# Kernel tuning notes

Hardware: AMD Instinct MI355X
Metric: run time of the kernel (lower is better)

## Reference

```python
import jax, jax.numpy as jnp
import numpy as np

N_NODES = 100000
N_EDGES = 1600000
D = 128

def setup_inputs() -> dict:
    key = jax.random.key(0)
    k1, k2, k3, k4 = jax.random.split(key, 4)
    x = jax.random.normal(k1, (N_NODES, D), dtype=jnp.float32)
    edge_index = jax.random.randint(k2, (2, N_EDGES), 0, N_NODES, dtype=jnp.int64)
    eps = jnp.zeros((1,), dtype=jnp.float32)
    W1 = jax.random.normal(k3, (D, D), dtype=jnp.float32) * (1.0 / np.sqrt(D))
    b1 = jnp.zeros((D,), dtype=jnp.float32)
    W2 = jax.random.normal(k4, (D, D), dtype=jnp.float32) * (1.0 / np.sqrt(D))
    b2 = jnp.zeros((D,), dtype=jnp.float32)
    return {"x": x, "edge_index": edge_index, "eps": eps,
            "W1": W1, "b1": b1, "W2": W2, "b2": b2}

def reference(x, edge_index, eps, W1, b1, W2, b2):
    src, dst = edge_index[0], edge_index[1]
    # spmm: sum of neighbor features h_j for each destination node i
    agg = jax.ops.segment_sum(x[src], dst, num_segments=N_NODES)  # [N, D]
    out = (1.0 + eps[0]) * x + agg
    # apply_func: 2-layer MLP (GIN paper)
    h = jax.nn.relu(out @ W1 + b1)
    return h @ W2 + b2
```

## Files before the change

### kernel.cpp

```cpp
#include <hip/hip_runtime.h>

#define D 128
#define BSHIFT 7
#define NSUB 8
#define SUBCAP 384
#define CAP 2560
#define LDSPITCH 136

#define NBMAX 784
#define LCAP 16
#define FCH 8

typedef __attribute__((ext_vector_type(8))) short bf16x8;
typedef __attribute__((ext_vector_type(4))) float f32x4;
typedef __attribute__((ext_vector_type(2))) float f32x2;
typedef __attribute__((ext_vector_type(4))) unsigned int u32x4;

__device__ __forceinline__ unsigned short f2bf(float f) {
    union { float f; unsigned int u; } c; c.f = f;
    return (unsigned short)((c.u + 0x7FFFu + ((c.u >> 16) & 1u)) >> 16);
}

__global__ __launch_bounds__(256) void conv_all(
    const float* __restrict__ x, unsigned short* __restrict__ xb,
    const float* __restrict__ W1, unsigned short* __restrict__ W1t,
    const float* __restrict__ W2, unsigned short* __restrict__ W2t,
    int* __restrict__ cur, int total4, int ncur)
{
    int gid = blockIdx.x * 256 + threadIdx.x;
    if (gid < total4) {
        float4 v = ((const float4*)x)[gid];
        ushort4 o;
        o.x = f2bf(v.x); o.y = f2bf(v.y); o.z = f2bf(v.z); o.w = f2bf(v.w);
        ((ushort4*)xb)[gid] = o;
        return;
    }
    int r = gid - total4;
    if (r < 16384) {
        int n = r >> 7, k = r & 127;
        W1t[n * 128 + k] = f2bf(W1[k * 128 + n]);
        return;
    }
    r -= 16384;
    if (r < 16384) {
        int n = r >> 7, k = r & 127;
        W2t[n * 128 + k] = f2bf(W2[k * 128 + n]);
        return;
    }
    r -= 16384;
    if (r < ncur) cur[r] = 0;
}

__global__ __launch_bounds__(512) void bin_kernel(
    const int* __restrict__ ei, int* __restrict__ cur,
    int* __restrict__ pairs, int E, int nbuck)
{
    __shared__ int lbuf[NBMAX * LCAP];
    __shared__ int lcnt[NBMAX];

    int tid = threadIdx.x;
    int slice = blockIdx.x & (NSUB - 1);
    int nblocks = gridDim.x;
    int epb = (E + nblocks - 1) / nblocks;
    int start = blockIdx.x * epb;
    int end = min(start + epb, E);

    for (int b = tid; b < nbuck; b += 512) lcnt[b] = 0;
    __syncthreads();

    for (int base = start; base < end; base += 512) {
        int gid = base + tid;
        if (gid < end) {
            int d = __builtin_nontemporal_load(&ei[E + gid]);
            int s = __builtin_nontemporal_load(&ei[gid]);
            int b = d >> BSHIFT;
            int val = ((d & 127) << 17) | s;
            int pos = atomicAdd(&lcnt[b], 1);
            if (pos < LCAP) {
                lbuf[b * LCAP + pos] = val;
            } else {
                int sb = b * NSUB + slice;
                int gp = atomicAdd(&cur[sb], 1);
                if (gp < SUBCAP) pairs[(size_t)sb * SUBCAP + gp] = val;
            }
        }
        __syncthreads();
        for (int b = tid; b < nbuck; b += 512) {
            int c = min(lcnt[b], LCAP);
            int nf = (c / FCH) * FCH;
            if (nf > 0) {
                int sb = b * NSUB + slice;
                int gbase = atomicAdd(&cur[sb], nf);
                int* dst = pairs + (size_t)sb * SUBCAP + gbase;
                if ((gbase & 3) == 0 && gbase + nf <= SUBCAP) {
                    #pragma unroll
                    for (int i = 0; i < LCAP; i += 4) {
                        if (i >= nf) break;
                        *(int4*)(dst + i) = *(int4*)(lbuf + b * LCAP + i);
                    }
                } else {
                    for (int i = 0; i < nf; ++i)
                        if (gbase + i < SUBCAP) dst[i] = lbuf[b * LCAP + i];
                }
                int rem = c - nf;
                for (int i = 0; i < rem; ++i)
                    lbuf[b * LCAP + i] = lbuf[b * LCAP + nf + i];
                lcnt[b] = rem;
            } else {
                lcnt[b] = c;
            }
        }
        __syncthreads();
    }

    for (int b = tid; b < nbuck; b += 512) {
        int c = min(lcnt[b], LCAP);
        if (c > 0) {
            int sb = b * NSUB + slice;
            int gbase = atomicAdd(&cur[sb], c);
            for (int i = 0; i < c; ++i)
                if (gbase + i < SUBCAP)
                    pairs[(size_t)sb * SUBCAP + gbase + i] = lbuf[b * LCAP + i];
        }
    }
}

__global__ __launch_bounds__(256) void local_fill(
    const int* __restrict__ cur, const int* __restrict__ pairs,
    int* __restrict__ csr, int* __restrict__ rs, int N)
{
    __shared__ int ldata[CAP];
    __shared__ int outsrc[CAP];
    __shared__ int lcnt[128], lofs[128], lincl[128];
    __shared__ int red[256];

    int b = blockIdx.x;
    int tid = threadIdx.x;
    int node0 = b << BSHIFT;

    int pacc = 0;
    for (int i = tid; i < b * NSUB; i += 256) pacc += min(cur[i], SUBCAP);
    red[tid] = pacc;
    __syncthreads();
    for (int s = 128; s > 0; s >>= 1) {
        if (tid < s) red[tid] += red[tid + s];
        __syncthreads();
    }
    int base = red[0];

    int off = 0;
    #pragma unroll
    for (int s = 0; s < NSUB; ++s) {
        int c = min(cur[b * NSUB + s], SUBCAP);
        const int* pp = pairs + (size_t)(b * NSUB + s) * SUBCAP;
        for (int i = tid; i < c && off + i < CAP; i += 256)
            ldata[off + i] = pp[i];
        off += c;
    }
    int cnt = min(off, CAP);
    __syncthreads();

    if (tid < 128) lcnt[tid] = 0;
    __syncthreads();
    for (int i = tid; i < cnt; i += 256)
        atomicAdd(&lcnt[ldata[i] >> 17], 1);
    __syncthreads();

    if (tid < 128) lincl[tid] = lcnt[tid];
    __syncthreads();
    for (int off2 = 1; off2 < 128; off2 <<= 1) {
        int t = 0;
        if (tid < 128 && tid >= off2) t = lincl[tid - off2];
        __syncthreads();
        if (tid < 128) lincl[tid] += t;
        __syncthreads();
    }
    if (tid < 128) lofs[tid] = lincl[tid] - lcnt[tid];
    __syncthreads();

    for (int i = tid; i < cnt; i += 256) {
        int v = ldata[i];
        int p = atomicAdd(&lofs[v >> 17], 1);
        outsrc[p] = v & 0x1FFFF;
    }
    __syncthreads();

    for (int i = tid; i < cnt; i += 256)
        csr[base + i] = outsrc[i];
    int nn = N - node0; if (nn > 128) nn = 128;
    if (tid < nn) rs[node0 + tid] = base + lincl[tid];
}

__global__ __launch_bounds__(256) void gather_kernel(
    const unsigned short* __restrict__ xb, const float* __restrict__ epsp,
    const int* __restrict__ rs, const int* __restrict__ csr,
    unsigned short* __restrict__ ub, int N)
{
    int sub  = threadIdx.x >> 5;
    int lane = threadIdx.x & 31;
    int hi   = lane >> 4;
    int c16  = lane & 15;
    int node = blockIdx.x * 8 + sub;
    if (node >= N) return;

    int start = (node == 0) ? 0 : rs[node - 1];
    int end   = rs[node];
    int boff  = c16 * 8;

    f32x2 acc[4];
    {
        float ep1 = 1.0f + epsp[0];
        u32x4 xr = *(const u32x4*)(xb + (size_t)node * D + boff);
        f32x2 z = {0.f, 0.f};
        #pragma unroll
        for (int e = 0; e < 4; ++e) {
            unsigned int w = xr[e];
            f32x2 t;
            t.x = __uint_as_float(w << 16);
            t.y = __uint_as_float(w & 0xFFFF0000u);
            acc[e] = hi ? z : (ep1 * t);
        }
    }

    #define ACC8(v)                                                         \
        {                                                                   \
            _Pragma("unroll")                                               \
            for (int e = 0; e < 4; ++e) {                                   \
                unsigned int w = (v)[e];                                    \
                f32x2 t;                                                    \
                t.x = __uint_as_float(w << 16);                             \
                t.y = __uint_as_float(w & 0xFFFF0000u);                     \
                acc[e] += t;                                                \
            }                                                               \
        }

    int j = start;
    for (; j + 16 <= end; j += 16) {
        int i0 = csr[j      + hi], i1 = csr[j +  2 + hi];
        int i2 = csr[j +  4 + hi], i3 = csr[j +  6 + hi];
        int i4 = csr[j +  8 + hi], i5 = csr[j + 10 + hi];
        int i6 = csr[j + 12 + hi], i7 = csr[j + 14 + hi];
        u32x4 v0 = *(const u32x4*)(xb + (size_t)i0 * D + boff);
        u32x4 v1 = *(const u32x4*)(xb + (size_t)i1 * D + boff);
        u32x4 v2 = *(const u32x4*)(xb + (size_t)i2 * D + boff);
        u32x4 v3 = *(const u32x4*)(xb + (size_t)i3 * D + boff);
        u32x4 v4 = *(const u32x4*)(xb + (size_t)i4 * D + boff);
        u32x4 v5 = *(const u32x4*)(xb + (size_t)i5 * D + boff);
        u32x4 v6 = *(const u32x4*)(xb + (size_t)i6 * D + boff);
        u32x4 v7 = *(const u32x4*)(xb + (size_t)i7 * D + boff);
        ACC8(v0); ACC8(v1); ACC8(v2); ACC8(v3);
        ACC8(v4); ACC8(v5); ACC8(v6); ACC8(v7);
    }
    if (j + 8 <= end) {
        int i0 = csr[j + hi],     i1 = csr[j + 2 + hi];
        int i2 = csr[j + 4 + hi], i3 = csr[j + 6 + hi];
        u32x4 v0 = *(const u32x4*)(xb + (size_t)i0 * D + boff);
        u32x4 v1 = *(const u32x4*)(xb + (size_t)i1 * D + boff);
        u32x4 v2 = *(const u32x4*)(xb + (size_t)i2 * D + boff);
        u32x4 v3 = *(const u32x4*)(xb + (size_t)i3 * D + boff);
        ACC8(v0); ACC8(v1); ACC8(v2); ACC8(v3);
        j += 8;
    }
    if (j < end) {
        int lim = end - 1;
        int e0 = j + hi, e1 = j + 2 + hi, e2 = j + 4 + hi, e3 = j + 6 + hi;
        int s0 = csr[min(e0, lim)], s1 = csr[min(e1, lim)];
        int s2 = csr[min(e2, lim)], s3 = csr[min(e3, lim)];
        u32x4 v0 = *(const u32x4*)(xb + (size_t)s0 * D + boff);
        u32x4 v1 = *(const u32x4*)(xb + (size_t)s1 * D + boff);
        u32x4 v2 = *(const u32x4*)(xb + (size_t)s2 * D + boff);
        u32x4 v3 = *(const u32x4*)(xb + (size_t)s3 * D + boff);
        unsigned int m0 = (e0 < end) ? 0xFFFFFFFFu : 0u;
        unsigned int m1 = (e1 < end) ? 0xFFFFFFFFu : 0u;
        unsigned int m2 = (e2 < end) ? 0xFFFFFFFFu : 0u;
        unsigned int m3 = (e3 < end) ? 0xFFFFFFFFu : 0u;
        #pragma unroll
        for (int e = 0; e < 4; ++e) { v0[e] &= m0; v1[e] &= m1; v2[e] &= m2; v3[e] &= m3; }
        ACC8(v0); ACC8(v1); ACC8(v2); ACC8(v3);
    }
    #undef ACC8

    #pragma unroll
    for (int e = 0; e < 4; ++e) {
        acc[e].x += __shfl_xor(acc[e].x, 16);
        acc[e].y += __shfl_xor(acc[e].y, 16);
    }

    if (hi == 0) {
        u32x4 o;
        #pragma unroll
        for (int e = 0; e < 4; ++e) {
            unsigned int lo = f2bf(acc[e].x);
            unsigned int hf = f2bf(acc[e].y);
            o[e] = lo | (hf << 16);
        }
        __builtin_nontemporal_store(o, (u32x4*)(ub + (size_t)node * D + boff));
    }
}

__global__ __launch_bounds__(256, 2) void mlp_fused(
    const unsigned short* __restrict__ in,
    const unsigned short* __restrict__ W1t, const float* __restrict__ b1,
    const unsigned short* __restrict__ W2t, const float* __restrict__ b2,
    float* __restrict__ out, int N)
{
    __shared__ unsigned short Wl[128 * LDSPITCH];
    __shared__ unsigned short Al[64 * LDSPITCH];

    int tid = threadIdx.x;
    int row0 = blockIdx.x * 64;
    int wave = tid >> 6, lane = tid & 63;
    int l16 = lane & 15, lq = lane >> 4;

    for (int i = tid; i < 128 * 16; i += 256) {
        int r = i >> 4, cc = i & 15;
        ((int4*)(Wl + r * LDSPITCH))[cc] = ((const int4*)(W1t + r * 128))[cc];
    }
    for (int i = tid; i < 64 * 16; i += 256) {
        int r = i >> 4, cc = i & 15;
        int4 v = make_int4(0, 0, 0, 0);
        if (row0 + r < N) v = ((const int4*)(in + (size_t)(row0 + r) * 128))[cc];
        ((int4*)(Al + r * LDSPITCH))[cc] = v;
    }
    __syncthreads();

    f32x4 acc[8];
    #pragma unroll
    for (int t = 0; t < 8; ++t) acc[t] = (f32x4){0.f, 0.f, 0.f, 0.f};

    int arow = wave * 16 + l16;
    #pragma unroll
    for (int kk = 0; kk < 4; ++kk) {
        int k0 = kk * 32 + lq * 8;
        bf16x8 a = *(const bf16x8*)(Al + arow * LDSPITCH + k0);
        #pragma unroll
        for (int t = 0; t < 8; ++t) {
            bf16x8 b = *(const bf16x8*)(Wl + (t * 16 + l16) * LDSPITCH + k0);
            acc[t] = __builtin_amdgcn_mfma_f32_16x16x32_bf16(a, b, acc[t], 0, 0, 0);
        }
    }
    __syncthreads();

    for (int i = tid; i < 128 * 16; i += 256) {
        int r = i >> 4, cc = i & 15;
        ((int4*)(Wl + r * LDSPITCH))[cc] = ((const int4*)(W2t + r * 128))[cc];
    }
    #pragma unroll
    for (int t = 0; t < 8; ++t) {
        int col = t * 16 + l16;
        float bv = b1[col];
        #pragma unroll
        for (int r = 0; r < 4; ++r) {
            int row = wave * 16 + lq * 4 + r;
            float v = fmaxf(acc[t][r] + bv, 0.0f);
            Al[row * LDSPITCH + col] = f2bf(v);
        }
    }
    __syncthreads();

    #pragma unroll
    for (int t = 0; t < 8; ++t) acc[t] = (f32x4){0.f, 0.f, 0.f, 0.f};
    #pragma unroll
    for (int kk = 0; kk < 4; ++kk) {
        int k0 = kk * 32 + lq * 8;
        bf16x8 a = *(const bf16x8*)(Al + arow * LDSPITCH + k0);
        #pragma unroll
        for (int t = 0; t < 8; ++t) {
            bf16x8 b = *(const bf16x8*)(Wl + (t * 16 + l16) * LDSPITCH + k0);
            acc[t] = __builtin_amdgcn_mfma_f32_16x16x32_bf16(a, b, acc[t], 0, 0, 0);
        }
    }

    #pragma unroll
    for (int t = 0; t < 8; ++t) {
        int col = t * 16 + l16;
        float bv = b2[col];
        #pragma unroll
        for (int r = 0; r < 4; ++r) {
            int row = row0 + wave * 16 + lq * 4 + r;
            if (row >= N) continue;
            out[(size_t)row * 128 + col] = acc[t][r] + bv;
        }
    }
}

extern "C" void kernel_launch(void* const* d_in, const int* in_sizes, int n_in,
                              void* d_out, int out_size, void* d_ws, size_t ws_size,
                              hipStream_t stream) {
    const float* x   = (const float*)d_in[0];
    const int*   ei  = (const int*)d_in[1];
    const float* eps = (const float*)d_in[2];
    const float* W1  = (const float*)d_in[3];
    const float* b1  = (const float*)d_in[4];
    const float* W2  = (const float*)d_in[5];
    const float* b2  = (const float*)d_in[6];
    float* out = (float*)d_out;

    int E = in_sizes[1] / 2;
    int N = in_sizes[0] / D;
    int nbuck = (N + 127) >> BSHIFT;
    int ncur = nbuck * NSUB;

    char* ws = (char*)d_ws;
    int* cur   = (int*)(ws);
    int* rs    = (int*)(ws + 32768);
    int* pairs = (int*)(ws + 434176);
    int* csr   = (int*)(ws + 10044416);
    unsigned short* xb  = (unsigned short*)(ws + 16445440);
    unsigned short* ub  = (unsigned short*)(ws + 42046464);
    unsigned short* W1t = (unsigned short*)(ws + 67647488);
    unsigned short* W2t = (unsigned short*)(ws + 67680256);

    int total4 = N * D / 4;
    int convtot = total4 + 32768 + ncur;
    conv_all<<<(convtot + 255) / 256, 256, 0, stream>>>(
        x, xb, W1, W1t, W2, W2t, cur, total4, ncur);

    bin_kernel<<<256, 512, 0, stream>>>(ei, cur, pairs, E, nbuck);
    local_fill<<<nbuck, 256, 0, stream>>>(cur, pairs, csr, rs, N);

    gather_kernel<<<(N + 7) / 8, 256, 0, stream>>>(xb, eps, rs, csr, ub, N);

    int gemm_blocks = (N + 63) / 64;
    mlp_fused<<<gemm_blocks, 256, 0, stream>>>(ub, W1t, b1, W2t, b2, out, N);
}
```

Before: 256.2 us.

## Fuse neighbor gather into MLP kernel and merge conversion with binning

The gather/aggregate stage now runs inside the MLP kernel: each block aggregates its 64 rows directly into LDS, so the bf16 intermediate no longer makes a round trip through global memory and one launch disappears. Separately, the x/weight bf16 conversion blocks are appended to the binning kernel's grid so both run concurrently, and zeroing the cursor array moves into its own tiny kernel. In exchange, the gather loop is unrolled less (8 instead of 16 edges per step), occupancy hints change to 3 blocks per CU, and the MFMA work now waits on serialized per-block gathers.

```diff
diff --git a/kernel.cpp b/kernel.cpp
--- a/kernel.cpp
+++ b/kernel.cpp
@@ -10,6 +10,7 @@
 #define NBMAX 784
 #define LCAP 16
 #define FCH 8
+#define NBIN 256
 
 typedef __attribute__((ext_vector_type(8))) short bf16x8;
 typedef __attribute__((ext_vector_type(4))) float f32x4;
@@ -21,47 +22,54 @@
     return (unsigned short)((c.u + 0x7FFFu + ((c.u >> 16) & 1u)) >> 16);
 }
 
-__global__ __launch_bounds__(256) void conv_all(
+__global__ __launch_bounds__(512) void zerocur(int* __restrict__ cur, int ncur)
+{
+    int gid = blockIdx.x * 512 + threadIdx.x;
+    if (gid < ncur) cur[gid] = 0;
+}
+
+__global__ __launch_bounds__(512) void conv_bin(
     const float* __restrict__ x, unsigned short* __restrict__ xb,
     const float* __restrict__ W1, unsigned short* __restrict__ W1t,
     const float* __restrict__ W2, unsigned short* __restrict__ W2t,
-    int* __restrict__ cur, int total4, int ncur)
-{
-    int gid = blockIdx.x * 256 + threadIdx.x;
-    if (gid < total4) {
-        float4 v = ((const float4*)x)[gid];
-        ushort4 o;
-        o.x = f2bf(v.x); o.y = f2bf(v.y); o.z = f2bf(v.z); o.w = f2bf(v.w);
-        ((ushort4*)xb)[gid] = o;
-        return;
-    }
-    int r = gid - total4;
-    if (r < 16384) {
-        int n = r >> 7, k = r & 127;
-        W1t[n * 128 + k] = f2bf(W1[k * 128 + n]);
-        return;
-    }
-    r -= 16384;
-    if (r < 16384) {
-        int n = r >> 7, k = r & 127;
-        W2t[n * 128 + k] = f2bf(W2[k * 128 + n]);
-        return;
-    }
-    r -= 16384;
-    if (r < ncur) cur[r] = 0;
-}
-
-__global__ __launch_bounds__(512) void bin_kernel(
     const int* __restrict__ ei, int* __restrict__ cur,
-    int* __restrict__ pairs, int E, int nbuck)
+    int* __restrict__ pairs, int E, int nbuck, int total4)
 {
     __shared__ int lbuf[NBMAX * LCAP];
     __shared__ int lcnt[NBMAX];
 
     int tid = threadIdx.x;
+
+    if (blockIdx.x >= NBIN) {
+        int base = (blockIdx.x - NBIN) * 1024 + tid;
+        #pragma unroll
+        for (int t = 0; t < 2; ++t) {
+            int gid = base + t * 512;
+            if (gid < total4) {
+                float4 v = ((const float4*)x)[gid];
+                ushort4 o;
+                o.x = f2bf(v.x); o.y = f2bf(v.y);
+                o.z = f2bf(v.z); o.w = f2bf(v.w);
+                ((ushort4*)xb)[gid] = o;
+            } else {
+                int r = gid - total4;
+                if (r < 16384) {
+                    int n = r >> 7, k = r & 127;
+                    W1t[n * 128 + k] = f2bf(W1[k * 128 + n]);
+                } else {
+                    r -= 16384;
+                    if (r < 16384) {
+                        int n = r >> 7, k = r & 127;
+                        W2t[n * 128 + k] = f2bf(W2[k * 128 + n]);
+                    }
+                }
+            }
+        }
+        return;
+    }
+
     int slice = blockIdx.x & (NSUB - 1);
-    int nblocks = gridDim.x;
-    int epb = (E + nblocks - 1) / nblocks;
+    int epb = (E + NBIN - 1) / NBIN;
     int start = blockIdx.x * epb;
     int end = min(start + epb, E);
 
@@ -191,115 +199,9 @@
     if (tid < nn) rs[node0 + tid] = base + lincl[tid];
 }
 
-__global__ __launch_bounds__(256) void gather_kernel(
+__global__ __launch_bounds__(256, 3) void mlp_gather(
     const unsigned short* __restrict__ xb, const float* __restrict__ epsp,
     const int* __restrict__ rs, const int* __restrict__ csr,
-    unsigned short* __restrict__ ub, int N)
-{
-    int sub  = threadIdx.x >> 5;
-    int lane = threadIdx.x & 31;
-    int hi   = lane >> 4;
-    int c16  = lane & 15;
-    int node = blockIdx.x * 8 + sub;
-    if (node >= N) return;
-
-    int start = (node == 0) ? 0 : rs[node - 1];
-    int end   = rs[node];
-    int boff  = c16 * 8;
-
-    f32x2 acc[4];
-    {
-        float ep1 = 1.0f + epsp[0];
-        u32x4 xr = *(const u32x4*)(xb + (size_t)node * D + boff);
-        f32x2 z = {0.f, 0.f};
-        #pragma unroll
-        for (int e = 0; e < 4; ++e) {
-            unsigned int w = xr[e];
-            f32x2 t;
-            t.x = __uint_as_float(w << 16);
-            t.y = __uint_as_float(w & 0xFFFF0000u);
-            acc[e] = hi ? z : (ep1 * t);
-        }
-    }
-
-    #define ACC8(v)                                                         \
-        {                                                                   \
-            _Pragma("unroll")                                               \
-            for (int e = 0; e < 4; ++e) {                                   \
-                unsigned int w = (v)[e];                                    \
-                f32x2 t;                                                    \
-                t.x = __uint_as_float(w << 16);                             \
-                t.y = __uint_as_float(w & 0xFFFF0000u);                     \
-                acc[e] += t;                                                \
-            }                                                               \
-        }
-
-    int j = start;
-    for (; j + 16 <= end; j += 16) {
-        int i0 = csr[j      + hi], i1 = csr[j +  2 + hi];
-        int i2 = csr[j +  4 + hi], i3 = csr[j +  6 + hi];
-        int i4 = csr[j +  8 + hi], i5 = csr[j + 10 + hi];
-        int i6 = csr[j + 12 + hi], i7 = csr[j + 14 + hi];
-        u32x4 v0 = *(const u32x4*)(xb + (size_t)i0 * D + boff);
-        u32x4 v1 = *(const u32x4*)(xb + (size_t)i1 * D + boff);
-        u32x4 v2 = *(const u32x4*)(xb + (size_t)i2 * D + boff);
-        u32x4 v3 = *(const u32x4*)(xb + (size_t)i3 * D + boff);
-        u32x4 v4 = *(const u32x4*)(xb + (size_t)i4 * D + boff);
-        u32x4 v5 = *(const u32x4*)(xb + (size_t)i5 * D + boff);
-        u32x4 v6 = *(const u32x4*)(xb + (size_t)i6 * D + boff);
-        u32x4 v7 = *(const u32x4*)(xb + (size_t)i7 * D + boff);
-        ACC8(v0); ACC8(v1); ACC8(v2); ACC8(v3);
-        ACC8(v4); ACC8(v5); ACC8(v6); ACC8(v7);
-    }
-    if (j + 8 <= end) {
-        int i0 = csr[j + hi],     i1 = csr[j + 2 + hi];
-        int i2 = csr[j + 4 + hi], i3 = csr[j + 6 + hi];
-        u32x4 v0 = *(const u32x4*)(xb + (size_t)i0 * D + boff);
-        u32x4 v1 = *(const u32x4*)(xb + (size_t)i1 * D + boff);
-        u32x4 v2 = *(const u32x4*)(xb + (size_t)i2 * D + boff);
-        u32x4 v3 = *(const u32x4*)(xb + (size_t)i3 * D + boff);
-        ACC8(v0); ACC8(v1); ACC8(v2); ACC8(v3);
-        j += 8;
-    }
-    if (j < end) {
-        int lim = end - 1;
-        int e0 = j + hi, e1 = j + 2 + hi, e2 = j + 4 + hi, e3 = j + 6 + hi;
-        int s0 = csr[min(e0, lim)], s1 = csr[min(e1, lim)];
-        int s2 = csr[min(e2, lim)], s3 = csr[min(e3, lim)];
-        u32x4 v0 = *(const u32x4*)(xb + (size_t)s0 * D + boff);
-        u32x4 v1 = *(const u32x4*)(xb + (size_t)s1 * D + boff);
-        u32x4 v2 = *(const u32x4*)(xb + (size_t)s2 * D + boff);
-        u32x4 v3 = *(const u32x4*)(xb + (size_t)s3 * D + boff);
-        unsigned int m0 = (e0 < end) ? 0xFFFFFFFFu : 0u;
-        unsigned int m1 = (e1 < end) ? 0xFFFFFFFFu : 0u;
-        unsigned int m2 = (e2 < end) ? 0xFFFFFFFFu : 0u;
-        unsigned int m3 = (e3 < end) ? 0xFFFFFFFFu : 0u;
-        #pragma unroll
-        for (int e = 0; e < 4; ++e) { v0[e] &= m0; v1[e] &= m1; v2[e] &= m2; v3[e] &= m3; }
-        ACC8(v0); ACC8(v1); ACC8(v2); ACC8(v3);
-    }
-    #undef ACC8
-
-    #pragma unroll
-    for (int e = 0; e < 4; ++e) {
-        acc[e].x += __shfl_xor(acc[e].x, 16);
-        acc[e].y += __shfl_xor(acc[e].y, 16);
-    }
-
-    if (hi == 0) {
-        u32x4 o;
-        #pragma unroll
-        for (int e = 0; e < 4; ++e) {
-            unsigned int lo = f2bf(acc[e].x);
-            unsigned int hf = f2bf(acc[e].y);
-            o[e] = lo | (hf << 16);
-        }
-        __builtin_nontemporal_store(o, (u32x4*)(ub + (size_t)node * D + boff));
-    }
-}
-
-__global__ __launch_bounds__(256, 2) void mlp_fused(
-    const unsigned short* __restrict__ in,
     const unsigned short* __restrict__ W1t, const float* __restrict__ b1,
     const unsigned short* __restrict__ W2t, const float* __restrict__ b2,
     float* __restrict__ out, int N)
@@ -309,20 +211,113 @@
 
     int tid = threadIdx.x;
     int row0 = blockIdx.x * 64;
-    int wave = tid >> 6, lane = tid & 63;
-    int l16 = lane & 15, lq = lane >> 4;
 
     for (int i = tid; i < 128 * 16; i += 256) {
         int r = i >> 4, cc = i & 15;
         ((int4*)(Wl + r * LDSPITCH))[cc] = ((const int4*)(W1t + r * 128))[cc];
     }
-    for (int i = tid; i < 64 * 16; i += 256) {
-        int r = i >> 4, cc = i & 15;
-        int4 v = make_int4(0, 0, 0, 0);
-        if (row0 + r < N) v = ((const int4*)(in + (size_t)(row0 + r) * 128))[cc];
-        ((int4*)(Al + r * LDSPITCH))[cc] = v;
-    }
-    __syncthreads();
+
+    {
+        int sub  = tid >> 5;
+        int lane = threadIdx.x & 31;
+        int hi   = lane >> 4;
+        int c16  = lane & 15;
+        int boff = c16 * 8;
+        float ep1 = 1.0f + epsp[0];
+
+        for (int nn = 0; nn < 8; ++nn) {
+            int r = nn * 8 + sub;
+            int node = row0 + r;
+            if (node >= N) {
+                if (hi == 0) {
+                    u32x4 z = {0u, 0u, 0u, 0u};
+                    *(u32x4*)(Al + r * LDSPITCH + boff) = z;
+                }
+                continue;
+            }
+            int start = (node == 0) ? 0 : rs[node - 1];
+            int end   = rs[node];
+
+            f32x2 acc[4];
+            {
+                u32x4 xr = *(const u32x4*)(xb + (size_t)node * D + boff);
+                f32x2 z2 = {0.f, 0.f};
+                #pragma unroll
+                for (int e = 0; e < 4; ++e) {
+                    unsigned int w = xr[e];
+                    f32x2 t;
+                    t.x = __uint_as_float(w << 16);
+                    t.y = __uint_as_float(w & 0xFFFF0000u);
+                    acc[e] = hi ? z2 : (ep1 * t);
+                }
+            }
+
+            #define ACC8(v)                                                 \
+                {                                                           \
+                    _Pragma("unroll")                                       \
+                    for (int e = 0; e < 4; ++e) {                           \
+                        unsigned int w = (v)[e];                            \
+                        f32x2 t;                                            \
+                        t.x = __uint_as_float(w << 16);                     \
+                        t.y = __uint_as_float(w & 0xFFFF0000u);             \
+                        acc[e] += t;                                        \
+                    }                                                       \
+                }
+
+            int j = start;
+            for (; j + 8 <= end; j += 8) {
+                int i0 = csr[j + hi],     i1 = csr[j + 2 + hi];
+                int i2 = csr[j + 4 + hi], i3 = csr[j + 6 + hi];
+                u32x4 v0 = *(const u32x4*)(xb + (size_t)i0 * D + boff);
+                u32x4 v1 = *(const u32x4*)(xb + (size_t)i1 * D + boff);
+                u32x4 v2 = *(const u32x4*)(xb + (size_t)i2 * D + boff);
+                u32x4 v3 = *(const u32x4*)(xb + (size_t)i3 * D + boff);
+                ACC8(v0); ACC8(v1); ACC8(v2); ACC8(v3);
+            }
+            if (j < end) {
+                int lim = end - 1;
+                int e0 = j + hi, e1 = j + 2 + hi;
+                int e2 = j + 4 + hi, e3 = j + 6 + hi;
+                int s0 = csr[min(e0, lim)], s1 = csr[min(e1, lim)];
+                int s2 = csr[min(e2, lim)], s3 = csr[min(e3, lim)];
+                u32x4 v0 = *(const u32x4*)(xb + (size_t)s0 * D + boff);
+                u32x4 v1 = *(const u32x4*)(xb + (size_t)s1 * D + boff);
+                u32x4 v2 = *(const u32x4*)(xb + (size_t)s2 * D + boff);
+                u32x4 v3 = *(const u32x4*)(xb + (size_t)s3 * D + boff);
+                unsigned int m0 = (e0 < end) ? 0xFFFFFFFFu : 0u;
+                unsigned int m1 = (e1 < end) ? 0xFFFFFFFFu : 0u;
+                unsigned int m2 = (e2 < end) ? 0xFFFFFFFFu : 0u;
+                unsigned int m3 = (e3 < end) ? 0xFFFFFFFFu : 0u;
+                #pragma unroll
+                for (int e = 0; e < 4; ++e) {
+                    v0[e] &= m0; v1[e] &= m1; v2[e] &= m2; v3[e] &= m3;
+                }
+                ACC8(v0); ACC8(v1); ACC8(v2); ACC8(v3);
+            }
+            #undef ACC8
+
+            #pragma unroll
+            for (int e = 0; e < 4; ++e) {
+                acc[e].x += __shfl_xor(acc[e].x, 16);
+                acc[e].y += __shfl_xor(acc[e].y, 16);
+            }
+
+            if (hi == 0) {
+                u32x4 o;
+                #pragma unroll
+                for (int e = 0; e < 4; ++e) {
+                    unsigned int lo = f2bf(acc[e].x);
+                    unsigned int hf = f2bf(acc[e].y);
+                    o[e] = lo | (hf << 16);
+                }
+                *(u32x4*)(Al + r * LDSPITCH + boff) = o;
+            }
+        }
+    }
+    __syncthreads();
+
+    int wave = tid >> 6, lane = tid & 63;
+    int l16 = lane & 15, lq = lane >> 4;
 
     f32x4 acc[8];
     #pragma unroll
@@ -407,20 +402,19 @@
     int* pairs = (int*)(ws + 434176);
     int* csr   = (int*)(ws + 10044416);
     unsigned short* xb  = (unsigned short*)(ws + 16445440);
-    unsigned short* ub  = (unsigned short*)(ws + 42046464);
     unsigned short* W1t = (unsigned short*)(ws + 67647488);
     unsigned short* W2t = (unsigned short*)(ws + 67680256);
 
     int total4 = N * D / 4;
-    int convtot = total4 + 32768 + ncur;
-    conv_all<<<(convtot + 255) / 256, 256, 0, stream>>>(
-        x, xb, W1, W1t, W2, W2t, cur, total4, ncur);
-
-    bin_kernel<<<256, 512, 0, stream>>>(ei, cur, pairs, E, nbuck);
+    int convitems = total4 + 32768;
+    int nconv = (convitems + 1023) / 1024;
+
+    zerocur<<<(ncur + 511) / 512, 512, 0, stream>>>(cur, ncur);
+    conv_bin<<<NBIN + nconv, 512, 0, stream>>>(
+        x, xb, W1, W1t, W2, W2t, ei, cur, pairs, E, nbuck, total4);
     local_fill<<<nbuck, 256, 0, stream>>>(cur, pairs, csr, rs, N);
 
-    gather_kernel<<<(N + 7) / 8, 256, 0, stream>>>(xb, eps, rs, csr, ub, N);
-
     int gemm_blocks = (N + 63) / 64;
-    mlp_fused<<<gemm_blocks, 256, 0, stream>>>(ub, W1t, b1, W2t, b2, out, N);
-}
+    mlp_gather<<<gemm_blocks, 256, 0, stream>>>(
+        xb, eps, rs, csr, W1t, b1, W2t, b2, out, N);
+}
```

New measurement: 256.5 us. Within noise of the previous version (+0.1%).
